# Performance work log

Measured on AMD Instinct MI355X. Metric: run time of the kernel, lower is better.

The kernel has to match this reference:

```python
import jax, jax.numpy as jnp
import numpy as np

ALIGN_SCALE = 3.0
UNIF_SCALE = 1.0
EPS = 1e-12  # torch F.normalize eps


def _normalize(x):
    n = jnp.linalg.norm(x, axis=-1, keepdims=True)
    return x / jnp.maximum(n, EPS)


def _unif_loss(a, b):
    # log(mean(exp(-2 * ||a_i - b_j||^2))) over all N*M pairs, fused via GEMM identity
    sq_a = jnp.sum(a * a, axis=1)  # [N]
    sq_b = jnp.sum(b * b, axis=1)  # [M]
    # squared distances: ||a||^2 + ||b||^2 - 2 a.b, clipped at 0 for numerics
    d2 = jnp.maximum(sq_a[:, None] + sq_b[None, :] - 2.0 * (a @ b.T), 0.0)  # [N, M]
    return jnp.log(jnp.mean(jnp.exp(-2.0 * d2)))


def setup_inputs() -> dict:
    key = jax.random.key(0)
    k1, k2 = jax.random.split(key)
    N, D = 8192, 512
    return {
        "image_embed": jax.random.normal(k1, (N, D), dtype=jnp.float32),
        "text_embed": jax.random.normal(k2, (N, D), dtype=jnp.float32),
    }


def reference(image_embed, text_embed):
    img = _normalize(image_embed)
    txt = _normalize(text_embed)
    # alignment: mean squared L2 between paired embeddings
    diff = img - txt
    align_loss = jnp.mean(jnp.sum(diff * diff, axis=1))
    # single device: gathered-all tensors equal the local tensors
    text_unif = _unif_loss(txt, txt)
    image_unif = _unif_loss(img, img)
    unif_loss = (text_unif + image_unif) / 2.0
    return ALIGN_SCALE * align_loss + UNIF_SCALE * unif_loss
```

## Files before the change

### kernel.cpp

```cpp
#include <hip/hip_runtime.h>
#include <hip/hip_bf16.h>


#define NROWS 8192
#define DBYTES 256
#define NTRI  2080
#define NJOBS 4160
#define GRAMBLK 512
#define SCALE4 0x7B7B7B7B

typedef __attribute__((ext_vector_type(8)))  int   int8v;
typedef __attribute__((ext_vector_type(4)))  int   int4v;
typedef __attribute__((ext_vector_type(16))) float float16v;

__device__ inline void load_lds16(const void* g, void* l) {
    __builtin_amdgcn_global_load_lds(
        (const __attribute__((address_space(1))) void*)g,
        (__attribute__((address_space(3))) void*)l, 16, 0, 0);
}

__device__ inline int swz(int r) { return (r ^ (r >> 3)) & 7; }

__device__ inline unsigned fp4_code(float x) {
    const float a = fabsf(x);
    unsigned c = (a < 0.25f) ? 0u : (a < 0.75f) ? 1u : (a < 1.25f) ? 2u :
                 (a < 1.75f) ? 3u : (a < 2.5f)  ? 4u : (a < 3.5f)  ? 5u :
                 (a < 5.0f)  ? 6u : 7u;
    return c | ((__float_as_uint(x) >> 28) & 8u);
}

__global__ __launch_bounds__(256) void normalize_kernel(
    const float* __restrict__ img, const float* __restrict__ txt,
    int* __restrict__ nimg, int* __restrict__ ntxt,
    float* __restrict__ alignp,
    float* __restrict__ S)
{
    if (blockIdx.x == 0 && threadIdx.x < 64) S[threadIdx.x] = 0.0f;

    const int lane = threadIdx.x & 63;
    const int wave = threadIdx.x >> 6;
    const int row  = blockIdx.x * 4 + wave;

    const float4* pi = (const float4*)(img + (size_t)row * 512);
    const float4* pt = (const float4*)(txt + (size_t)row * 512);
    const float4 i0 = pi[2 * lane], i1 = pi[2 * lane + 1];
    const float4 t0 = pt[2 * lane], t1 = pt[2 * lane + 1];

    float ssi = i0.x*i0.x + i0.y*i0.y + i0.z*i0.z + i0.w*i0.w
              + i1.x*i1.x + i1.y*i1.y + i1.z*i1.z + i1.w*i1.w;
    float sst = t0.x*t0.x + t0.y*t0.y + t0.z*t0.z + t0.w*t0.w
              + t1.x*t1.x + t1.y*t1.y + t1.z*t1.z + t1.w*t1.w;
    float dot = i0.x*t0.x + i0.y*t0.y + i0.z*t0.z + i0.w*t0.w
              + i1.x*t1.x + i1.y*t1.y + i1.z*t1.z + i1.w*t1.w;

    #pragma unroll
    for (int off = 1; off < 64; off <<= 1) {
        ssi += __shfl_xor(ssi, off);
        sst += __shfl_xor(sst, off);
        dot += __shfl_xor(dot, off);
    }
    const float inv_i = 1.0f / fmaxf(sqrtf(ssi), 1e-12f);
    const float inv_t = 1.0f / fmaxf(sqrtf(sst), 1e-12f);
    const float si = 16.0f * inv_i;
    const float st = 16.0f * inv_t;

    unsigned wi = 0, wt = 0;
    wi |= fp4_code(i0.x * si)       | (fp4_code(i0.y * si) << 4)
       |  (fp4_code(i0.z * si) << 8)| (fp4_code(i0.w * si) << 12)
       |  (fp4_code(i1.x * si) <<16)| (fp4_code(i1.y * si) << 20)
       |  (fp4_code(i1.z * si) <<24)| (fp4_code(i1.w * si) << 28);
    wt |= fp4_code(t0.x * st)       | (fp4_code(t0.y * st) << 4)
       |  (fp4_code(t0.z * st) << 8)| (fp4_code(t0.w * st) << 12)
       |  (fp4_code(t1.x * st) <<16)| (fp4_code(t1.y * st) << 20)
       |  (fp4_code(t1.z * st) <<24)| (fp4_code(t1.w * st) << 28);

    nimg[row * 64 + lane] = (int)wi;
    ntxt[row * 64 + lane] = (int)wt;

    __shared__ float r4[4];
    if (lane == 0) r4[wave] = dot * inv_i * inv_t;
    __syncthreads();
    if (threadIdx.x == 0)
        alignp[blockIdx.x] = r4[0] + r4[1] + r4[2] + r4[3];
}

__device__ inline void decode_job(int t,
        const unsigned char* __restrict__ A0,
        const unsigned char* __restrict__ A1,
        const unsigned char*& pA, const unsigned char*& pB,
        float& w0, float& w1)
{
    const int m  = (t >= NTRI) ? 1 : 0;
    const int tt = t - m * NTRI;
    int i = (int)((129.0f - sqrtf(16641.0f - 8.0f * (float)tt)) * 0.5f);
    while (64 * (i + 1) - ((i + 1) * i) / 2 <= tt) ++i;
    while (64 * i - (i * (i - 1)) / 2 > tt) --i;
    const int j = i + (tt - (64 * i - (i * (i - 1)) / 2));
    const unsigned char* M = m ? A1 : A0;
    pA = M + (size_t)i * 128 * DBYTES;
    pB = M + (size_t)j * 128 * DBYTES;
    const float w = (j > i) ? 2.0f : 1.0f;
    w0 = m ? 0.0f : w;
    w1 = m ? w : 0.0f;
}

__device__ inline void stage_tile(const unsigned char* __restrict__ pA,
                                  const unsigned char* __restrict__ pB,
                                  int k0, unsigned char* lA, unsigned char* lB,
                                  int tid)
{
    #pragma unroll
    for (int rnd = 0; rnd < 4; ++rnd) {
        const int slot = rnd * 4096 + tid * 16;
        const int r    = slot >> 7;
        const int cp   = (slot >> 4) & 7;
        const int cl   = cp ^ swz(r);
        load_lds16(pA + (size_t)r * DBYTES + k0 + cl * 16, lA + slot);
    }
    #pragma unroll
    for (int rnd = 0; rnd < 4; ++rnd) {
        const int slot = rnd * 4096 + tid * 16;
        const int r    = slot >> 7;
        const int cp   = (slot >> 4) & 7;
        const int cl   = cp ^ swz(r);
        load_lds16(pB + (size_t)r * DBYTES + k0 + cl * 16, lB + slot);
    }
}

__global__ __launch_bounds__(256, 2) void gram_kernel(
    const unsigned char* __restrict__ A0,
    const unsigned char* __restrict__ A1,
    float* __restrict__ S)
{
    const int tid  = threadIdx.x;
    const int lane = tid & 63;
    const int wave = tid >> 6;
    const int wm = wave & 1, wn = wave >> 1;
    const int lr = lane & 31;
    const int h  = lane >> 5;
    const int b  = blockIdx.x;

    __shared__ __align__(16) unsigned char ldsA[2][128 * 128];
    __shared__ __align__(16) unsigned char ldsB[2][128 * 128];
    __shared__ float ps[4][2];

    const int J = (NJOBS - 1 - b) / GRAMBLK + 1;
    const int U = 2 * J;

    float16v acc[2][2];
    #pragma unroll
    for (int a = 0; a < 2; ++a)
        #pragma unroll
        for (int c = 0; c < 2; ++c)
            #pragma unroll
            for (int r = 0; r < 16; ++r) acc[a][c][r] = 0.0f;
    float s0 = 0.0f, s1 = 0.0f;

    const unsigned char *nA, *nB;
    float nw0, nw1;
    decode_job(b, A0, A1, nA, nB, nw0, nw1);
    float cw0 = nw0, cw1 = nw1;
    stage_tile(nA, nB, 0, ldsA[0], ldsB[0], tid);

    for (int u = 0; u < U; ++u) {
        const int buf = u & 1;
        if (u + 1 < U) {
            const int v = u + 1;
            if ((v & 1) == 0)
                decode_job(b + GRAMBLK * (v >> 1), A0, A1, nA, nB, nw0, nw1);
            stage_tile(nA, nB, (v & 1) * 128, ldsA[v & 1], ldsB[v & 1], tid);
            asm volatile("s_waitcnt vmcnt(8)" ::: "memory");
        } else {
            asm volatile("s_waitcnt vmcnt(0)" ::: "memory");
        }
        __builtin_amdgcn_sched_barrier(0);
        __builtin_amdgcn_s_barrier();
        __builtin_amdgcn_sched_barrier(0);

        const unsigned char* lA = ldsA[buf];
        const unsigned char* lB = ldsB[buf];
        #pragma unroll
        for (int kk = 0; kk < 4; ++kk) {
            const int c0 = kk * 2 + h;
            int8v av[2], bv[2];
            #pragma unroll
            for (int mt = 0; mt < 2; ++mt) {
                const int r = wm * 64 + mt * 32 + lr;
                *((int4v*)&av[mt]) =
                    *(const int4v*)&lA[r * 128 + (c0 ^ swz(r)) * 16];
                *((int4v*)&av[mt] + 1) = (int4v){0, 0, 0, 0};
            }
            #pragma unroll
            for (int nt = 0; nt < 2; ++nt) {
                const int r = wn * 64 + nt * 32 + lr;
                *((int4v*)&bv[nt]) =
                    *(const int4v*)&lB[r * 128 + (c0 ^ swz(r)) * 16];
                *((int4v*)&bv[nt] + 1) = (int4v){0, 0, 0, 0};
            }
            #pragma unroll
            for (int mt = 0; mt < 2; ++mt)
                #pragma unroll
                for (int nt = 0; nt < 2; ++nt)
                    acc[mt][nt] = __builtin_amdgcn_mfma_scale_f32_32x32x64_f8f6f4(
                        av[mt], bv[nt], acc[mt][nt],
                        4, 4,
                        0, SCALE4,
                        0, SCALE4);
        }

        if (u & 1) {
            float f = 0.0f;
            #pragma unroll
            for (int mt = 0; mt < 2; ++mt)
                #pragma unroll
                for (int nt = 0; nt < 2; ++nt)
                    #pragma unroll
                    for (int r2 = 0; r2 < 16; ++r2) {
                        const float g = acc[mt][nt][r2];
                        f += __expf(4.0f * fminf(g, 1.0f) - 4.0f);
                        acc[mt][nt][r2] = 0.0f;
                    }
            s0 += cw0 * f;
            s1 += cw1 * f;
            cw0 = nw0;  cw1 = nw1;
        }

        __builtin_amdgcn_sched_barrier(0);
        __builtin_amdgcn_s_barrier();
    }

    #pragma unroll
    for (int off = 32; off; off >>= 1) {
        s0 += __shfl_down(s0, off);
        s1 += __shfl_down(s1, off);
    }
    if (lane == 0) { ps[wave][0] = s0; ps[wave][1] = s1; }
    __syncthreads();
    if (tid == 0) {
        atomicAdd(&S[b & 31],        ps[0][0] + ps[1][0] + ps[2][0] + ps[3][0]);
        atomicAdd(&S[32 + (b & 31)], ps[0][1] + ps[1][1] + ps[2][1] + ps[3][1]);
    }
}

__global__ __launch_bounds__(256) void finalize_kernel(
    const float* __restrict__ S,
    const float* __restrict__ alignp,
    float* __restrict__ out)
{
    const int tid = threadIdx.x;
    float a = 0.0f;
    #pragma unroll
    for (int k = 0; k < 8; ++k) a += alignp[tid + 256 * k];
    #pragma unroll
    for (int off = 32; off; off >>= 1) a += __shfl_down(a, off);
    __shared__ float r4[4];
    if ((tid & 63) == 0) r4[tid >> 6] = a;
    __syncthreads();
    if (tid == 0) {
        const double A = (double)r4[0] + r4[1] + r4[2] + r4[3];
        double si = 0.0, st = 0.0;
        for (int k = 0; k < 32; ++k) { si += S[k]; st += S[32 + k]; }
        const double align = 2.0 - 2.0 * A / (double)NROWS;
        const double n2 = (double)NROWS * (double)NROWS;
        const double unif = 0.5 * (log(si / n2) + log(st / n2));
        out[0] = (float)(3.0 * align + unif);
    }
}

extern "C" void kernel_launch(void* const* d_in, const int* in_sizes, int n_in,
                              void* d_out, int out_size, void* d_ws, size_t ws_size,
                              hipStream_t stream) {
    const float* img = (const float*)d_in[0];
    const float* txt = (const float*)d_in[1];
    char* ws = (char*)d_ws;
    int* nimg = (int*)ws;
    int* ntxt = (int*)(ws + (size_t)NROWS * DBYTES);
    float* S      = (float*)(ws + 2 * (size_t)NROWS * DBYTES);
    float* alignp = S + 64;

    normalize_kernel<<<NROWS / 4, 256, 0, stream>>>(img, txt, nimg, ntxt, alignp, S);
    gram_kernel<<<GRAMBLK, 256, 0, stream>>>((const unsigned char*)nimg,
                                             (const unsigned char*)ntxt, S);
    finalize_kernel<<<1, 256, 0, stream>>>(S, alignp, (float*)d_out);
}
```

Baseline: 115.1 us.

## Interleave next-tile LDS prefetch with MFMA k-steps and raise MFMA priority

The whole-tile prefetch before compute is replaced by one pair of global-to-LDS loads issued inside each of the four k-steps, so memory traffic is spread across the MFMA work. Workgroup barriers are added around each k-step's LDS reads and MFMAs, giving a ping-pong style schedule. The MFMA block is also wrapped in s_setprio so its issue is favoured. Each iteration now has many more barriers, and the shortened waitcnt(2) bound together with the buffer reuse timing has to stay correct.

```diff
diff --git a/kernel.cpp b/kernel.cpp
--- a/kernel.cpp
+++ b/kernel.cpp
@@ -104,29 +104,6 @@
     w1 = m ? w : 0.0f;
 }
 
-__device__ inline void stage_tile(const unsigned char* __restrict__ pA,
-                                  const unsigned char* __restrict__ pB,
-                                  int k0, unsigned char* lA, unsigned char* lB,
-                                  int tid)
-{
-    #pragma unroll
-    for (int rnd = 0; rnd < 4; ++rnd) {
-        const int slot = rnd * 4096 + tid * 16;
-        const int r    = slot >> 7;
-        const int cp   = (slot >> 4) & 7;
-        const int cl   = cp ^ swz(r);
-        load_lds16(pA + (size_t)r * DBYTES + k0 + cl * 16, lA + slot);
-    }
-    #pragma unroll
-    for (int rnd = 0; rnd < 4; ++rnd) {
-        const int slot = rnd * 4096 + tid * 16;
-        const int r    = slot >> 7;
-        const int cp   = (slot >> 4) & 7;
-        const int cl   = cp ^ swz(r);
-        load_lds16(pB + (size_t)r * DBYTES + k0 + cl * 16, lB + slot);
-    }
-}
-
 __global__ __launch_bounds__(256, 2) void gram_kernel(
     const unsigned char* __restrict__ A0,
     const unsigned char* __restrict__ A1,
@@ -160,29 +137,49 @@
     float nw0, nw1;
     decode_job(b, A0, A1, nA, nB, nw0, nw1);
     float cw0 = nw0, cw1 = nw1;
-    stage_tile(nA, nB, 0, ldsA[0], ldsB[0], tid);
+    #pragma unroll
+    for (int rnd = 0; rnd < 4; ++rnd) {
+        const int slot = rnd * 4096 + tid * 16;
+        const int r    = slot >> 7;
+        const int cp   = (slot >> 4) & 7;
+        const int cl   = cp ^ swz(r);
+        load_lds16(nA + (size_t)r * DBYTES + cl * 16, &ldsA[0][slot]);
+        load_lds16(nB + (size_t)r * DBYTES + cl * 16, &ldsB[0][slot]);
+    }
 
     for (int u = 0; u < U; ++u) {
-        const int buf = u & 1;
-        if (u + 1 < U) {
-            const int v = u + 1;
-            if ((v & 1) == 0)
-                decode_job(b + GRAMBLK * (v >> 1), A0, A1, nA, nB, nw0, nw1);
-            stage_tile(nA, nB, (v & 1) * 128, ldsA[v & 1], ldsB[v & 1], tid);
-            asm volatile("s_waitcnt vmcnt(8)" ::: "memory");
-        } else {
-            asm volatile("s_waitcnt vmcnt(0)" ::: "memory");
-        }
-        __builtin_amdgcn_sched_barrier(0);
-        __builtin_amdgcn_s_barrier();
-        __builtin_amdgcn_sched_barrier(0);
-
+        const int buf  = u & 1;
+        const int v    = u + 1;
+        const bool more = (v < U);
+        if (more && ((v & 1) == 0))
+            decode_job(b + GRAMBLK * (v >> 1), A0, A1, nA, nB, nw0, nw1);
+        const int k0n  = (v & 1) * 128;
+        const int nbuf = v & 1;
         const unsigned char* lA = ldsA[buf];
         const unsigned char* lB = ldsB[buf];
+
         #pragma unroll
         for (int kk = 0; kk < 4; ++kk) {
+            if (more) {
+                const int slot = kk * 4096 + tid * 16;
+                const int r    = slot >> 7;
+                const int cp   = (slot >> 4) & 7;
+                const int cl   = cp ^ swz(r);
+                load_lds16(nA + (size_t)r * DBYTES + k0n + cl * 16,
+                           &ldsA[nbuf][slot]);
+                load_lds16(nB + (size_t)r * DBYTES + k0n + cl * 16,
+                           &ldsB[nbuf][slot]);
+            }
+
+            int8v av[2], bv[2];
             const int c0 = kk * 2 + h;
-            int8v av[2], bv[2];
+            if (kk == 0) {
+                if (more) asm volatile("s_waitcnt vmcnt(2)" ::: "memory");
+                else      asm volatile("s_waitcnt vmcnt(0)" ::: "memory");
+                __builtin_amdgcn_sched_barrier(0);
+                __builtin_amdgcn_s_barrier();
+                __builtin_amdgcn_sched_barrier(0);
+            }
             #pragma unroll
             for (int mt = 0; mt < 2; ++mt) {
                 const int r = wm * 64 + mt * 32 + lr;
@@ -197,6 +194,13 @@
                     *(const int4v*)&lB[r * 128 + (c0 ^ swz(r)) * 16];
                 *((int4v*)&bv[nt] + 1) = (int4v){0, 0, 0, 0};
             }
+            if (kk != 0) {
+                __builtin_amdgcn_sched_barrier(0);
+                __builtin_amdgcn_s_barrier();
+                __builtin_amdgcn_sched_barrier(0);
+            }
+
+            __builtin_amdgcn_s_setprio(1);
             #pragma unroll
             for (int mt = 0; mt < 2; ++mt)
                 #pragma unroll
@@ -206,6 +210,10 @@
                         4, 4,
                         0, SCALE4,
                         0, SCALE4);
+            __builtin_amdgcn_s_setprio(0);
+            __builtin_amdgcn_sched_barrier(0);
+            __builtin_amdgcn_s_barrier();
+            __builtin_amdgcn_sched_barrier(0);
         }
 
         if (u & 1) {
@@ -224,9 +232,6 @@
             s1 += cw1 * f;
             cw0 = nw0;  cw1 = nw1;
         }
-
-        __builtin_amdgcn_sched_barrier(0);
-        __builtin_amdgcn_s_barrier();
     }
 
     #pragma unroll
```

Result: slower. 120.1 us (+4.3%).
